# Optimization experiments

Measured on AMD Instinct MI355X. Metric: run time of the kernel, lower is better.

## Reference

```python
import jax, jax.numpy as jnp
import numpy as np

N_TARGETS = 6
RADIUS = 2
RECLEN = 2 * RADIUS + 1  # 5
SWAP_RC = True


def setup_inputs() -> dict:
    key = jax.random.key(0)
    heatmap = jax.random.uniform(key, (128, 1, 512, 512), dtype=jnp.float32)
    return {"heatmap": heatmap}


def _sample_one(hm):
    # hm: [H, W]. Iteratively: avg-pool (VALID), take first (row-major) argmax
    # of the pooled map, zero the corresponding RECLEN x RECLEN window, repeat.
    H, W = hm.shape
    pw = W - RECLEN + 1  # pooled width

    def step(hm, _):
        # sum-pool == avg-pool up to a positive constant -> same argmax
        agg = jax.lax.reduce_window(
            hm, 0.0, jax.lax.add,
            window_dimensions=(RECLEN, RECLEN),
            window_strides=(1, 1), padding='VALID')
        idx = jnp.argmax(agg)  # first occurrence, row-major (matches torch nonzero()[0])
        r = idx // pw
        c = idx % pw
        # suppress the window in the ORIGINAL heatmap (pooled index i -> window [i, i+RECLEN))
        hm = jax.lax.dynamic_update_slice(
            hm, jnp.zeros((RECLEN, RECLEN), hm.dtype), (r, c))
        return hm, jnp.stack([r + RADIUS, c + RADIUS])

    _, coords = jax.lax.scan(step, hm, None, length=N_TARGETS)
    return coords  # [N_TARGETS, 2] int


def reference(heatmap):
    # heatmap: [B, 1, H, W]
    coords = jax.vmap(_sample_one)(heatmap[:, 0])  # [B, N_TARGETS, 2] as (row, col)
    if SWAP_RC:
        coords = coords[:, :, ::-1]  # (col, row)
    return coords
```

## Files before the change

### kernel.cpp

```cpp
#include <hip/hip_runtime.h>
#include <hip/hip_bf16.h>

#define HM_W 512
#define HM_H 512
#define PW   508

__device__ __forceinline__ void load_row8(const float* __restrict__ hm, int y, int c0, float v[8]) {
    const float4* rp = reinterpret_cast<const float4*>(hm + y * HM_W + c0);
    float4 a = rp[0];
    float4 b = rp[1];
    v[0]=a.x; v[1]=a.y; v[2]=a.z; v[3]=a.w;
    v[4]=b.x; v[5]=b.y; v[6]=b.z; v[7]=b.w;
}

__device__ __forceinline__ void row_best_shfl(const float s[8], int lane, float& bv, int& bc) {
    float cb[12];
#pragma unroll
    for (int j = 0; j < 8; ++j) cb[j] = s[j];
#pragma unroll
    for (int j = 0; j < 4; ++j) cb[8 + j] = __shfl_down(s[j], 1);
    bv = -__builtin_inff();
    bc = 0x7fffffff;
    int c0 = lane * 8;
#pragma unroll
    for (int j = 0; j < 8; ++j) {
        int c = c0 + j;
        float w = cb[j] + cb[j + 1] + cb[j + 2] + cb[j + 3] + cb[j + 4];
        if (c < PW && w > bv) { bv = w; bc = c; }
    }
#pragma unroll
    for (int m = 1; m < 64; m <<= 1) {
        float ov = __shfl_xor(bv, m);
        int   oc = __shfl_xor(bc, m);
        if (ov > bv || (ov == bv && oc < bc)) { bv = ov; bc = oc; }
    }
}

__global__ void phase1_kernel(const float* __restrict__ hm_all,
                              float* __restrict__ rowv_ws, int* __restrict__ rowc_ws) {
    int b = blockIdx.y;
    int wave = threadIdx.x >> 6;
    int lane = threadIdx.x & 63;
    int c0 = lane * 8;
    const float* hm = hm_all + (size_t)b * HM_W * HM_H;

    int rbase = (blockIdx.x * 4 + wave) * 16;
    if (rbase >= PW) return;

    float w0[8], w1[8], w2[8], w3[8], w4[8];
    load_row8(hm, rbase + 0, c0, w0);
    load_row8(hm, rbase + 1, c0, w1);
    load_row8(hm, rbase + 2, c0, w2);
    load_row8(hm, rbase + 3, c0, w3);

#pragma unroll
    for (int rr = 0; rr < 16; ++rr) {
        int y = rbase + rr;
        if (y >= PW) break;
        load_row8(hm, y + 4, c0, w4);
        float s[8];
#pragma unroll
        for (int j = 0; j < 8; ++j)
            s[j] = ((((w0[j] + w1[j]) + w2[j]) + w3[j]) + w4[j]);
        float bv; int bc;
        row_best_shfl(s, lane, bv, bc);
        if (lane == 0) {
            rowv_ws[b * 512 + y] = bv;
            rowc_ws[b * 512 + y] = bc;
        }
#pragma unroll
        for (int j = 0; j < 8; ++j) { w0[j] = w1[j]; w1[j] = w2[j]; w2[j] = w3[j]; w3[j] = w4[j]; }
    }
}

__global__ void __launch_bounds__(1024) phase2_kernel(const float* __restrict__ hm_all,
                              const float* __restrict__ rowv_ws,
                              const int* __restrict__ rowc_ws,
                              int* __restrict__ out) {
    int b = blockIdx.x;
    const float* hm = hm_all + (size_t)b * HM_W * HM_H;
    int t = threadIdx.x;
    int wave = t >> 6, lane = t & 63;
    int c0 = lane * 8;

    __shared__ float rowv[512];
    __shared__ int   rowc[512];

    if (t < 512) {
        if (t < PW) { rowv[t] = rowv_ws[b * 512 + t]; rowc[t] = rowc_ws[b * 512 + t]; }
        else        { rowv[t] = -__builtin_inff();    rowc[t] = 0; }
    }

    int zrr[6], zcc[6];

#pragma unroll
    for (int it = 0; it < 6; ++it) {
        __syncthreads();

        float bv = -__builtin_inff(); int bi = 0x7fffffff;
#pragma unroll
        for (int j = 0; j < 8; ++j) {
            int idx = j * 64 + lane;
            float v = rowv[idx];
            if (v > bv) { bv = v; bi = idx; }
        }
#pragma unroll
        for (int m = 1; m < 64; m <<= 1) {
            float ov = __shfl_xor(bv, m);
            int   oi = __shfl_xor(bi, m);
            if (ov > bv || (ov == bv && oi < bi)) { bv = ov; bi = oi; }
        }
        int fr = bi;
        int fc = rowc[fr];
        zrr[it] = fr; zcc[it] = fc;
        if (t == 0) {
            out[b * 12 + it * 2 + 0] = fc + 2;
            out[b * 12 + it * 2 + 1] = fr + 2;
        }
        if (it == 5) break;

        __syncthreads();

        int y0 = fr - 4 < 0 ? 0 : fr - 4;
        int y1 = fr + 4 > PW - 1 ? PW - 1 : fr + 4;
        int y  = y0 + wave;
        if (wave < 9 && y <= y1) {
            float s[8];
#pragma unroll
            for (int j = 0; j < 8; ++j) s[j] = 0.f;
#pragma unroll
            for (int i = 0; i < 5; ++i) {
                float v[8];
                load_row8(hm, y + i, c0, v);
#pragma unroll
                for (int j = 0; j < 8; ++j) {
                    float vv = v[j];
#pragma unroll
                    for (int k = 0; k < 6; ++k) {
                        if (k <= it && (unsigned)(y + i - zrr[k]) < 5u
                                    && (unsigned)(c0 + j - zcc[k]) < 5u)
                            vv = 0.f;
                    }
                    s[j] += vv;
                }
            }
            float nv; int nc;
            row_best_shfl(s, lane, nv, nc);
            if (lane == 0) { rowv[y] = nv; rowc[y] = nc; }
        }
    }
}

extern "C" void kernel_launch(void* const* d_in, const int* in_sizes, int n_in,
                              void* d_out, int out_size, void* d_ws, size_t ws_size,
                              hipStream_t stream) {
    const float* hm = (const float*)d_in[0];
    int* out = (int*)d_out;
    float* rowv_ws = (float*)d_ws;
    int*   rowc_ws = (int*)((char*)d_ws + (size_t)128 * 512 * sizeof(float));

    phase1_kernel<<<dim3(8, 128), dim3(256), 0, stream>>>(hm, rowv_ws, rowc_ws);
    phase2_kernel<<<dim3(128), dim3(1024), 0, stream>>>(hm, rowv_ws, rowc_ws, out);
}
```

Measured before the change: 56.13 us.

## Keep per-row maxima in registers and cut phase-2 barriers; widen phase-1 row strips

Phase 2 now has every wave hold a private register copy of the 512 row maxima and their columns, so each wave does the argmax with no shared-memory read and no barrier before it. Only the 9 recomputed rows go through a small double-buffered shared array, leaving one barrier per iteration. The block shrinks to 576 threads (9 waves). Phase 1 gives each wave 32 rows instead of 16 and halves its grid, so fewer rows are reloaded for window overlap, but fewer blocks run in parallel.

```diff
diff --git a/kernel.cpp b/kernel.cpp
--- a/kernel.cpp
+++ b/kernel.cpp
@@ -44,7 +44,7 @@
     int c0 = lane * 8;
     const float* hm = hm_all + (size_t)b * HM_W * HM_H;
 
-    int rbase = (blockIdx.x * 4 + wave) * 16;
+    int rbase = (blockIdx.x * 4 + wave) * 32;
     if (rbase >= PW) return;
 
     float w0[8], w1[8], w2[8], w3[8], w4[8];
@@ -54,7 +54,7 @@
     load_row8(hm, rbase + 3, c0, w3);
 
 #pragma unroll
-    for (int rr = 0; rr < 16; ++rr) {
+    for (int rr = 0; rr < 32; ++rr) {
         int y = rbase + rr;
         if (y >= PW) break;
         load_row8(hm, y + 4, c0, w4);
@@ -73,7 +73,7 @@
     }
 }
 
-__global__ void __launch_bounds__(1024) phase2_kernel(const float* __restrict__ hm_all,
+__global__ void __launch_bounds__(576) phase2_kernel(const float* __restrict__ hm_all,
                               const float* __restrict__ rowv_ws,
                               const int* __restrict__ rowc_ws,
                               int* __restrict__ out) {
@@ -83,35 +83,34 @@
     int wave = t >> 6, lane = t & 63;
     int c0 = lane * 8;
 
-    __shared__ float rowv[512];
-    __shared__ int   rowc[512];
+    __shared__ float updv[2][9];
+    __shared__ int   updc[2][9];
 
-    if (t < 512) {
-        if (t < PW) { rowv[t] = rowv_ws[b * 512 + t]; rowc[t] = rowc_ws[b * 512 + t]; }
-        else        { rowv[t] = -__builtin_inff();    rowc[t] = 0; }
+    float rv[8]; int rc[8];
+#pragma unroll
+    for (int j = 0; j < 8; ++j) {
+        int idx = j * 64 + lane;
+        if (idx < PW) { rv[j] = rowv_ws[b * 512 + idx]; rc[j] = rowc_ws[b * 512 + idx]; }
+        else          { rv[j] = -__builtin_inff();      rc[j] = 0; }
     }
 
     int zrr[6], zcc[6];
 
 #pragma unroll
     for (int it = 0; it < 6; ++it) {
-        __syncthreads();
-
-        float bv = -__builtin_inff(); int bi = 0x7fffffff;
+        float bv = rv[0]; int bi = lane; int bc = rc[0];
 #pragma unroll
-        for (int j = 0; j < 8; ++j) {
-            int idx = j * 64 + lane;
-            float v = rowv[idx];
-            if (v > bv) { bv = v; bi = idx; }
+        for (int j = 1; j < 8; ++j) {
+            if (rv[j] > bv) { bv = rv[j]; bi = j * 64 + lane; bc = rc[j]; }
         }
 #pragma unroll
         for (int m = 1; m < 64; m <<= 1) {
             float ov = __shfl_xor(bv, m);
             int   oi = __shfl_xor(bi, m);
-            if (ov > bv || (ov == bv && oi < bi)) { bv = ov; bi = oi; }
+            int   oc = __shfl_xor(bc, m);
+            if (ov > bv || (ov == bv && oi < bi)) { bv = ov; bi = oi; bc = oc; }
         }
-        int fr = bi;
-        int fc = rowc[fr];
+        int fr = bi, fc = bc;
         zrr[it] = fr; zcc[it] = fc;
         if (t == 0) {
             out[b * 12 + it * 2 + 0] = fc + 2;
@@ -119,12 +118,12 @@
         }
         if (it == 5) break;
 
-        __syncthreads();
-
         int y0 = fr - 4 < 0 ? 0 : fr - 4;
         int y1 = fr + 4 > PW - 1 ? PW - 1 : fr + 4;
-        int y  = y0 + wave;
-        if (wave < 9 && y <= y1) {
+        int buf = it & 1;
+
+        int y = y0 + wave;
+        if (y <= y1) {
             float s[8];
 #pragma unroll
             for (int j = 0; j < 8; ++j) s[j] = 0.f;
@@ -146,7 +145,22 @@
             }
             float nv; int nc;
             row_best_shfl(s, lane, nv, nc);
-            if (lane == 0) { rowv[y] = nv; rowc[y] = nc; }
+            if (lane == 0) { updv[buf][wave] = nv; updc[buf][wave] = nc; }
+        }
+
+        __syncthreads();
+
+        int n = y1 - y0;
+#pragma unroll
+        for (int u = 0; u < 9; ++u) {
+            if (u <= n) {
+                float nv = updv[buf][u]; int ncol = updc[buf][u];
+                int yy = y0 + u;
+                int jj = yy >> 6, ll = yy & 63;
+#pragma unroll
+                for (int j = 0; j < 8; ++j)
+                    if (j == jj && lane == ll) { rv[j] = nv; rc[j] = ncol; }
+            }
         }
     }
 }
@@ -159,6 +173,6 @@
     float* rowv_ws = (float*)d_ws;
     int*   rowc_ws = (int*)((char*)d_ws + (size_t)128 * 512 * sizeof(float));
 
-    phase1_kernel<<<dim3(8, 128), dim3(256), 0, stream>>>(hm, rowv_ws, rowc_ws);
-    phase2_kernel<<<dim3(128), dim3(1024), 0, stream>>>(hm, rowv_ws, rowc_ws, out);
+    phase1_kernel<<<dim3(4, 128), dim3(256), 0, stream>>>(hm, rowv_ws, rowc_ws);
+    phase2_kernel<<<dim3(128), dim3(576), 0, stream>>>(hm, rowv_ws, rowc_ws, out);
 }
```

Result: slower. 76.34 us (+36.0%).

## Speculatively pick two non-overlapping peaks per iteration with double-buffered row updates

Applied to the files above, without the earlier changes.

Phase 2 now takes a second candidate peak in the same pass when it lies more than 8 rows away from the first and beats every row the first suppression touches, so one iteration can accept two peaks. Recomputed row maxima go into a double-buffered shared scratch, and the main row arrays are merged lazily on the next pass, which removes one barrier per iteration. The aim is fewer serial argmax/recompute rounds and fewer __syncthreads. In exchange there is extra overlay logic on every shared read, and the block shrinks to 640 threads with two recompute rows per wave.

```diff
diff --git a/kernel.cpp b/kernel.cpp
--- a/kernel.cpp
+++ b/kernel.cpp
@@ -73,7 +73,7 @@
     }
 }
 
-__global__ void __launch_bounds__(1024) phase2_kernel(const float* __restrict__ hm_all,
+__global__ void __launch_bounds__(640) phase2_kernel(const float* __restrict__ hm_all,
                               const float* __restrict__ rowv_ws,
                               const int* __restrict__ rowc_ws,
                               int* __restrict__ out) {
@@ -85,6 +85,8 @@
 
     __shared__ float rowv[512];
     __shared__ int   rowc[512];
+    __shared__ float updv[2][18];
+    __shared__ int   updc[2][18];
 
     if (t < 512) {
         if (t < PW) { rowv[t] = rowv_ws[b * 512 + t]; rowc[t] = rowc_ws[b * 512 + t]; }
@@ -92,62 +94,146 @@
     }
 
     int zrr[6], zcc[6];
-
-#pragma unroll
-    for (int it = 0; it < 6; ++it) {
+    int py0a = -1000, pna = 0, py0b = -1000, pnb = 0;
+    int cbuf = 0;
+    int npk = 0;
+
+    while (npk < 6) {
         __syncthreads();
-
-        float bv = -__builtin_inff(); int bi = 0x7fffffff;
+        int pbuf = cbuf ^ 1;
+
+        float bv1 = -__builtin_inff(); int bi1 = 0x7fffffff;
 #pragma unroll
         for (int j = 0; j < 8; ++j) {
             int idx = j * 64 + lane;
             float v = rowv[idx];
-            if (v > bv) { bv = v; bi = idx; }
+            unsigned ua = (unsigned)(idx - py0a);
+            if (ua < (unsigned)pna) v = updv[pbuf][ua];
+            unsigned ub = (unsigned)(idx - py0b);
+            if (ub < (unsigned)pnb) v = updv[pbuf][pna + ub];
+            if (v > bv1) { bv1 = v; bi1 = idx; }
         }
 #pragma unroll
         for (int m = 1; m < 64; m <<= 1) {
-            float ov = __shfl_xor(bv, m);
-            int   oi = __shfl_xor(bi, m);
-            if (ov > bv || (ov == bv && oi < bi)) { bv = ov; bi = oi; }
-        }
-        int fr = bi;
-        int fc = rowc[fr];
-        zrr[it] = fr; zcc[it] = fc;
+            float ov = __shfl_xor(bv1, m);
+            int   oi = __shfl_xor(bi1, m);
+            if (ov > bv1 || (ov == bv1 && oi < bi1)) { bv1 = ov; bi1 = oi; }
+        }
+        int fr1 = bi1;
+        int fc1 = rowc[fr1];
+        {
+            unsigned ua = (unsigned)(fr1 - py0a);
+            if (ua < (unsigned)pna) fc1 = updc[pbuf][ua];
+            unsigned ub = (unsigned)(fr1 - py0b);
+            if (ub < (unsigned)pnb) fc1 = updc[pbuf][pna + ub];
+        }
+#pragma unroll
+        for (int k = 0; k < 6; ++k) if (k == npk) { zrr[k] = fr1; zcc[k] = fc1; }
         if (t == 0) {
-            out[b * 12 + it * 2 + 0] = fc + 2;
-            out[b * 12 + it * 2 + 1] = fr + 2;
-        }
-        if (it == 5) break;
-
-        __syncthreads();
-
-        int y0 = fr - 4 < 0 ? 0 : fr - 4;
-        int y1 = fr + 4 > PW - 1 ? PW - 1 : fr + 4;
-        int y  = y0 + wave;
-        if (wave < 9 && y <= y1) {
-            float s[8];
-#pragma unroll
-            for (int j = 0; j < 8; ++j) s[j] = 0.f;
-#pragma unroll
-            for (int i = 0; i < 5; ++i) {
-                float v[8];
-                load_row8(hm, y + i, c0, v);
-#pragma unroll
-                for (int j = 0; j < 8; ++j) {
-                    float vv = v[j];
-#pragma unroll
-                    for (int k = 0; k < 6; ++k) {
-                        if (k <= it && (unsigned)(y + i - zrr[k]) < 5u
-                                    && (unsigned)(c0 + j - zcc[k]) < 5u)
-                            vv = 0.f;
+            out[b * 12 + npk * 2 + 0] = fc1 + 2;
+            out[b * 12 + npk * 2 + 1] = fr1 + 2;
+        }
+
+        if (t < 18) {
+            if (t < pna) {
+                rowv[py0a + t] = updv[pbuf][t]; rowc[py0a + t] = updc[pbuf][t];
+            } else if (t - pna < pnb) {
+                int yy = py0b + (t - pna);
+                rowv[yy] = updv[pbuf][t]; rowc[yy] = updc[pbuf][t];
+            }
+        }
+
+        int zlo = fr1 - 4 < 0 ? 0 : fr1 - 4;
+        int zhi = fr1 + 4 > PW - 1 ? PW - 1 : fr1 + 4;
+        int zn  = zhi - zlo + 1;
+
+        float Vz = -__builtin_inff();
+#pragma unroll
+        for (int k = 0; k < 9; ++k) {
+            if (k < zn) {
+                int yy = zlo + k;
+                float v = rowv[yy];
+                unsigned ua = (unsigned)(yy - py0a);
+                if (ua < (unsigned)pna) v = updv[pbuf][ua];
+                unsigned ub = (unsigned)(yy - py0b);
+                if (ub < (unsigned)pnb) v = updv[pbuf][pna + ub];
+                Vz = v > Vz ? v : Vz;
+            }
+        }
+
+        float bv2 = -__builtin_inff(); int bi2 = 0x7fffffff;
+#pragma unroll
+        for (int j = 0; j < 8; ++j) {
+            int idx = j * 64 + lane;
+            float v = rowv[idx];
+            unsigned ua = (unsigned)(idx - py0a);
+            if (ua < (unsigned)pna) v = updv[pbuf][ua];
+            unsigned ub = (unsigned)(idx - py0b);
+            if (ub < (unsigned)pnb) v = updv[pbuf][pna + ub];
+            if ((unsigned)(idx - zlo) < (unsigned)zn) v = -__builtin_inff();
+            if (v > bv2) { bv2 = v; bi2 = idx; }
+        }
+#pragma unroll
+        for (int m = 1; m < 64; m <<= 1) {
+            float ov = __shfl_xor(bv2, m);
+            int   oi = __shfl_xor(bi2, m);
+            if (ov > bv2 || (ov == bv2 && oi < bi2)) { bv2 = ov; bi2 = oi; }
+        }
+        int fr2 = bi2;
+        bool acc = (npk < 5) && (bv2 > Vz) && (fr2 > fr1 + 8 || fr2 < fr1 - 8);
+        if (acc) {
+            int fc2 = rowc[fr2];
+            unsigned ua = (unsigned)(fr2 - py0a);
+            if (ua < (unsigned)pna) fc2 = updc[pbuf][ua];
+            unsigned ub = (unsigned)(fr2 - py0b);
+            if (ub < (unsigned)pnb) fc2 = updc[pbuf][pna + ub];
+#pragma unroll
+            for (int k = 0; k < 6; ++k) if (k == npk + 1) { zrr[k] = fr2; zcc[k] = fc2; }
+            if (t == 0) {
+                out[b * 12 + (npk + 1) * 2 + 0] = fc2 + 2;
+                out[b * 12 + (npk + 1) * 2 + 1] = fr2 + 2;
+            }
+        }
+        int newn = npk + (acc ? 2 : 1);
+        if (newn >= 6) break;
+
+        int y0b = fr2 - 4 < 0 ? 0 : fr2 - 4;
+        int y1b = fr2 + 4 > PW - 1 ? PW - 1 : fr2 + 4;
+        int na = zn;
+        int nb = acc ? (y1b - y0b + 1) : 0;
+#pragma unroll
+        for (int p = 0; p < 2; ++p) {
+            int li = wave + p * 10;
+            if (li < na + nb) {
+                int y = (li < na) ? (zlo + li) : (y0b + (li - na));
+                float s[8];
+#pragma unroll
+                for (int j = 0; j < 8; ++j) s[j] = 0.f;
+#pragma unroll
+                for (int i = 0; i < 5; ++i) {
+                    float v[8];
+                    load_row8(hm, y + i, c0, v);
+#pragma unroll
+                    for (int j = 0; j < 8; ++j) {
+                        float vv = v[j];
+#pragma unroll
+                        for (int k = 0; k < 6; ++k) {
+                            if (k < newn && (unsigned)(y + i - zrr[k]) < 5u
+                                         && (unsigned)(c0 + j - zcc[k]) < 5u)
+                                vv = 0.f;
+                        }
+                        s[j] += vv;
                     }
-                    s[j] += vv;
                 }
-            }
-            float nv; int nc;
-            row_best_shfl(s, lane, nv, nc);
-            if (lane == 0) { rowv[y] = nv; rowc[y] = nc; }
-        }
+                float nv; int nc;
+                row_best_shfl(s, lane, nv, nc);
+                if (lane == 0) { updv[cbuf][li] = nv; updc[cbuf][li] = nc; }
+            }
+        }
+
+        py0a = zlo; pna = na; py0b = y0b; pnb = nb;
+        cbuf ^= 1;
+        npk = newn;
     }
 }
 
@@ -160,5 +246,5 @@
     int*   rowc_ws = (int*)((char*)d_ws + (size_t)128 * 512 * sizeof(float));
 
     phase1_kernel<<<dim3(8, 128), dim3(256), 0, stream>>>(hm, rowv_ws, rowc_ws);
-    phase2_kernel<<<dim3(128), dim3(1024), 0, stream>>>(hm, rowv_ws, rowc_ws, out);
-}
+    phase2_kernel<<<dim3(128), dim3(640), 0, stream>>>(hm, rowv_ws, rowc_ws, out);
+}
```

After: 80.39 us. +43.2%, slower.

## Overlap window recompute with masked argmax in phase2 using double-buffered updates

Applied to the files above, without the earlier changes.

Phase2 now runs the recomputation of the nine affected pooled rows (waves 0-8) at the same time as a tenth wave that takes the argmax over all rows not touched by the previous suppression. The two results are merged through small double-buffered shared arrays, so each iteration needs one barrier instead of two. The block shrinks from 1024 to 640 threads, and the zero-masking check is restructured to test the row condition once per row instead of once per element. The cost is extra shared-memory bookkeeping and a more intricate merge and tie-breaking path.

```diff
diff --git a/kernel.cpp b/kernel.cpp
--- a/kernel.cpp
+++ b/kernel.cpp
@@ -73,7 +73,7 @@
     }
 }
 
-__global__ void __launch_bounds__(1024) phase2_kernel(const float* __restrict__ hm_all,
+__global__ void __launch_bounds__(640) phase2_kernel(const float* __restrict__ hm_all,
                               const float* __restrict__ rowv_ws,
                               const int* __restrict__ rowc_ws,
                               int* __restrict__ out) {
@@ -85,18 +85,22 @@
 
     __shared__ float rowv[512];
     __shared__ int   rowc[512];
+    __shared__ float updv[2][9];
+    __shared__ int   updc[2][9];
+    __shared__ float obv[2];
+    __shared__ int   obr[2], obc[2];
 
     if (t < 512) {
         if (t < PW) { rowv[t] = rowv_ws[b * 512 + t]; rowc[t] = rowc_ws[b * 512 + t]; }
         else        { rowv[t] = -__builtin_inff();    rowc[t] = 0; }
     }
+    __syncthreads();
 
     int zrr[6], zcc[6];
-
-#pragma unroll
-    for (int it = 0; it < 6; ++it) {
-        __syncthreads();
-
+    int pz0 = 0, pzn = 0;
+    int fr, fc;
+
+    {
         float bv = -__builtin_inff(); int bi = 0x7fffffff;
 #pragma unroll
         for (int j = 0; j < 8; ++j) {
@@ -110,44 +114,101 @@
             int   oi = __shfl_xor(bi, m);
             if (ov > bv || (ov == bv && oi < bi)) { bv = ov; bi = oi; }
         }
-        int fr = bi;
-        int fc = rowc[fr];
-        zrr[it] = fr; zcc[it] = fc;
+        fr = bi; fc = rowc[fr];
+    }
+    zrr[0] = fr; zcc[0] = fc;
+    if (t == 0) {
+        out[b * 12 + 0] = fc + 2;
+        out[b * 12 + 1] = fr + 2;
+    }
+
+#pragma unroll
+    for (int it = 0; it < 5; ++it) {
+        int wbuf = it & 1;
+        int rbuf = wbuf ^ 1;
+
+        int zlo = fr - 4 < 0 ? 0 : fr - 4;
+        int zhi = fr + 4 > PW - 1 ? PW - 1 : fr + 4;
+        int zn  = zhi - zlo + 1;
+
+        if (t < 9 && t < pzn) {
+            rowv[pz0 + t] = updv[rbuf][t];
+            rowc[pz0 + t] = updc[rbuf][t];
+        }
+
+        if (wave < 9) {
+            if (wave < zn) {
+                int y = zlo + wave;
+                float s[8];
+#pragma unroll
+                for (int j = 0; j < 8; ++j) s[j] = 0.f;
+#pragma unroll
+                for (int i = 0; i < 5; ++i) {
+                    float v[8];
+                    load_row8(hm, y + i, c0, v);
+#pragma unroll
+                    for (int k = 0; k < 6; ++k) {
+                        if (k <= it) {
+                            if ((unsigned)(y + i - zrr[k]) < 5u) {
+#pragma unroll
+                                for (int j = 0; j < 8; ++j)
+                                    if ((unsigned)(c0 + j - zcc[k]) < 5u) v[j] = 0.f;
+                            }
+                        }
+                    }
+#pragma unroll
+                    for (int j = 0; j < 8; ++j) s[j] += v[j];
+                }
+                float nv; int nc;
+                row_best_shfl(s, lane, nv, nc);
+                if (lane == 0) { updv[wbuf][wave] = nv; updc[wbuf][wave] = nc; }
+            }
+        } else {
+            float bv = -__builtin_inff(); int bi = 0x7fffffff;
+#pragma unroll
+            for (int j = 0; j < 8; ++j) {
+                int idx = j * 64 + lane;
+                float v = rowv[idx];
+                unsigned u = (unsigned)(idx - pz0);
+                if (u < (unsigned)pzn) v = updv[rbuf][u];
+                if ((unsigned)(idx - zlo) < (unsigned)zn) v = -__builtin_inff();
+                if (v > bv) { bv = v; bi = idx; }
+            }
+#pragma unroll
+            for (int m = 1; m < 64; m <<= 1) {
+                float ov = __shfl_xor(bv, m);
+                int   oi = __shfl_xor(bi, m);
+                if (ov > bv || (ov == bv && oi < bi)) { bv = ov; bi = oi; }
+            }
+            if (lane == 0) {
+                int bc2 = rowc[bi];
+                unsigned u = (unsigned)(bi - pz0);
+                if (u < (unsigned)pzn) bc2 = updc[rbuf][u];
+                obv[wbuf] = bv; obr[wbuf] = bi; obc[wbuf] = bc2;
+            }
+        }
+
+        __syncthreads();
+
+        {
+            float bv = obv[wbuf]; int br = obr[wbuf]; int bc2 = obc[wbuf];
+#pragma unroll
+            for (int u = 0; u < 9; ++u) {
+                if (u < zn) {
+                    int yy = zlo + u;
+                    float v = updv[wbuf][u];
+                    if (v > bv || (v == bv && yy < br)) { bv = v; br = yy; bc2 = updc[wbuf][u]; }
+                }
+            }
+            fr = br; fc = bc2;
+        }
+        zrr[it + 1] = fr; zcc[it + 1] = fc;
         if (t == 0) {
-            out[b * 12 + it * 2 + 0] = fc + 2;
-            out[b * 12 + it * 2 + 1] = fr + 2;
-        }
-        if (it == 5) break;
-
-        __syncthreads();
-
-        int y0 = fr - 4 < 0 ? 0 : fr - 4;
-        int y1 = fr + 4 > PW - 1 ? PW - 1 : fr + 4;
-        int y  = y0 + wave;
-        if (wave < 9 && y <= y1) {
-            float s[8];
-#pragma unroll
-            for (int j = 0; j < 8; ++j) s[j] = 0.f;
-#pragma unroll
-            for (int i = 0; i < 5; ++i) {
-                float v[8];
-                load_row8(hm, y + i, c0, v);
-#pragma unroll
-                for (int j = 0; j < 8; ++j) {
-                    float vv = v[j];
-#pragma unroll
-                    for (int k = 0; k < 6; ++k) {
-                        if (k <= it && (unsigned)(y + i - zrr[k]) < 5u
-                                    && (unsigned)(c0 + j - zcc[k]) < 5u)
-                            vv = 0.f;
-                    }
-                    s[j] += vv;
-                }
-            }
-            float nv; int nc;
-            row_best_shfl(s, lane, nv, nc);
-            if (lane == 0) { rowv[y] = nv; rowc[y] = nc; }
-        }
+            out[b * 12 + (it + 1) * 2 + 0] = fc + 2;
+            out[b * 12 + (it + 1) * 2 + 1] = fr + 2;
+        }
+
+        pz0 = zlo; pzn = zn;
     }
 }
 
@@ -160,5 +221,5 @@
     int*   rowc_ws = (int*)((char*)d_ws + (size_t)128 * 512 * sizeof(float));
 
     phase1_kernel<<<dim3(8, 128), dim3(256), 0, stream>>>(hm, rowv_ws, rowc_ws);
-    phase2_kernel<<<dim3(128), dim3(1024), 0, stream>>>(hm, rowv_ws, rowc_ws, out);
-}
+    phase2_kernel<<<dim3(128), dim3(640), 0, stream>>>(hm, rowv_ws, rowc_ws, out);
+}
```

Measured after the change: 50.89 us, median of 2. 9.3% less time.
